# Optimization experiments

Hardware: AMD Instinct MI355X
Metric: run time of the kernel (lower is better)

The kernel has to match this reference:

```python
import jax, jax.numpy as jnp
import numpy as np

DIM = 256; HEADS = 8; HD = DIM // HEADS; WIN = 3; LOCAL = WIN * WIN
SR = 8; SHARED = 4; ROUTED = 2
B = 4; RES = 64; TBL = 4096
EPS = 1.1920929e-07  # torch.finfo(float32).eps


def _l2(x):
    return x / jnp.clip(jnp.linalg.norm(x, axis=-1, keepdims=True), EPS)


def _forward(x, relative_coords_table, q_w, q_b, kv_w, kv_b, temperature,
             query_embedding, rpb_local, learnable_tokens, learnable_bias,
             cpb1_w, cpb1_b, cpb2_w, cpb2_b, sr_w, sr_b, norm_g, norm_b,
             wg_w, wg0_w, wg1_w, proj_w, proj_b, relative_pos_index, H, W):
    B_, N, C = x.shape
    pH, pW = H // SR, W // SR
    PL = pH * pW
    _x = x.reshape(B_ * N, C)

    # ---- MoE head routing: top-k gating over routed heads ----
    gates = jax.nn.softmax(_x @ wg_w.T, axis=1)                 # (BN, n_routed)
    _, idx = jax.lax.top_k(gates, ROUTED)
    mask = jax.nn.one_hot(idx, gates.shape[1], dtype=gates.dtype).sum(axis=1)
    rg = gates * mask
    rg = rg / jnp.clip(jnp.sum(rg, axis=1, keepdims=True), EPS)
    routed_gates = rg.reshape(B_, N, -1) * ROUTED

    # ---- seq-length-scale buffer: log(local valid-window count + pool_len) ----
    r = WIN // 2
    ch = np.minimum(np.arange(H) + r, H - 1) - np.maximum(np.arange(H) - r, 0) + 1
    cw = np.minimum(np.arange(W) + r, W - 1) - np.maximum(np.arange(W) - r, 0) + 1
    sls = jnp.asarray(np.log(np.outer(ch, cw).reshape(-1, 1).astype(np.float32) + PL))

    # ---- queries ----
    q = (x @ q_w.T + q_b).reshape(B_, N, HEADS, HD).transpose(0, 2, 1, 3)
    q_norm = _l2(q)                                             # (B,h,N,d)
    q_scaled = (q_norm + query_embedding) * jax.nn.softplus(temperature) * sls

    # ---- local branch: unfold normalized k and v over 3x3 windows (zero pad) ----
    kv = x @ kv_w.T + kv_b                                      # (B,N,2C)
    k_loc = _l2(kv[..., :C].reshape(B_, N, HEADS, HD)).reshape(B_, N, C)
    kvl = jnp.concatenate([k_loc, kv[..., C:]], -1).transpose(0, 2, 1).reshape(B_, 2 * C, H, W)
    kvp = jnp.pad(kvl, ((0, 0), (0, 0), (r, r), (r, r)))
    patches = jnp.stack([kvp[:, :, i:i + H, j:j + W] for i in range(WIN) for j in range(WIN)], axis=2)
    patches = patches.reshape(B_, 2 * HEADS, HD, LOCAL, N).transpose(0, 1, 4, 2, 3)  # (B,2h,N,d,L)
    k_local, v_local = patches[:, :HEADS], patches[:, HEADS:]

    attn_local = jnp.einsum('bhnd,bhndl->bhnl', q_scaled, k_local) + rpb_local[:, None, :]

    # ---- pooled global branch ----
    x_ = x.transpose(0, 2, 1).reshape(B_, C, H, W)
    x_ = jnp.einsum('oc,bchw->bohw', sr_w, x_) + sr_b[None, :, None, None]  # 1x1 conv
    x_ = jax.nn.gelu(x_, approximate=False)
    x_ = x_.reshape(B_, C, pH, SR, pW, SR).mean((3, 5)).reshape(B_, C, PL).transpose(0, 2, 1)
    mu = x_.mean(-1, keepdims=True)
    var = ((x_ - mu) ** 2).mean(-1, keepdims=True)
    x_ = (x_ - mu) / jnp.sqrt(var + 1e-5) * norm_g + norm_b
    kvp2 = (x_ @ kv_w.T + kv_b).reshape(B_, PL, 2 * HEADS, HD).transpose(0, 2, 1, 3)
    k_pool, v_pool = kvp2[:, :HEADS], kvp2[:, HEADS:]

    cpb = jax.nn.relu(relative_coords_table @ cpb1_w.T + cpb1_b) @ cpb2_w.T + cpb2_b  # (T,h)
    pool_bias = cpb.T[:, relative_pos_index.reshape(-1)].reshape(HEADS, N, PL)
    attn_pool = jnp.einsum('bhnd,bhpd->bhnp', q_scaled, _l2(k_pool)) + pool_bias

    # ---- joint softmax over local + pooled keys ----
    attn = jax.nn.softmax(jnp.concatenate([attn_local, attn_pool], axis=-1), axis=-1)
    a_loc, a_pool = attn[..., :LOCAL], attn[..., LOCAL:]
    a_loc = jnp.einsum('bhnd,hdl->bhnl', q_norm, learnable_tokens) + learnable_bias + a_loc
    x_local = jnp.einsum('bhnl,bhndl->bhnd', a_loc, v_local)
    x_pool = jnp.einsum('bhnp,bhpd->bhnd', a_pool, v_pool)
    out = (x_local + x_pool).transpose(0, 2, 1, 3)              # (B,N,h,d)

    # ---- combine shared + routed head gates ----
    shared_gates = jax.nn.softmax(_x @ wg1_w.T, axis=1).reshape(B_, N, SHARED) * SHARED
    w0 = jax.nn.softmax(_x @ wg0_w.T, axis=1).reshape(B_, N, 2) * 2
    masked = jnp.concatenate([w0[..., 0:1] * shared_gates, w0[..., 1:2] * routed_gates], axis=-1)
    out = (masked[..., None] * out).reshape(B_, N, C)
    return out @ proj_w.T + proj_b


def setup_inputs() -> dict:
    key = jax.random.key(0)
    ks = jax.random.split(key, 20)
    H = W = RES
    N = H * W
    C = DIM
    PL = (H // SR) * (W // SR)

    def nrm(i, shape, s=0.02):
        return jax.random.normal(ks[i], shape, dtype=jnp.float32) * s

    return {
        'x': jax.random.normal(ks[0], (B, N, C), dtype=jnp.float32),
        'relative_coords_table': jax.random.normal(ks[1], (TBL, 2), dtype=jnp.float32),
        'q_w': nrm(3, (C, C)), 'q_b': jnp.zeros((C,), jnp.float32),
        'kv_w': nrm(4, (2 * C, C)), 'kv_b': jnp.zeros((2 * C,), jnp.float32),
        'temperature': jnp.full((HEADS, 1, 1), float(np.log(np.exp(1 / 0.24) - 1)), jnp.float32),
        'query_embedding': nrm(5, (HEADS, 1, HD)),
        'rpb_local': nrm(6, (HEADS, LOCAL), 0.0004),
        'learnable_tokens': nrm(7, (HEADS, HD, LOCAL)),
        'learnable_bias': jnp.zeros((HEADS, 1, LOCAL), jnp.float32),
        'cpb1_w': nrm(8, (512, 2)), 'cpb1_b': jnp.zeros((512,), jnp.float32),
        'cpb2_w': nrm(9, (HEADS, 512)), 'cpb2_b': jnp.zeros((HEADS,), jnp.float32),
        'sr_w': nrm(10, (C, C)), 'sr_b': jnp.zeros((C,), jnp.float32),
        'norm_g': jnp.ones((C,), jnp.float32), 'norm_b': jnp.zeros((C,), jnp.float32),
        'wg_w': nrm(11, (HEADS - SHARED, C)),
        'wg0_w': nrm(12, (2, C)),
        'wg1_w': nrm(13, (SHARED, C)),
        'proj_w': nrm(14, (C, C)), 'proj_b': jnp.zeros((C,), jnp.float32),
        'relative_pos_index': jax.random.randint(ks[2], (N, PL), 0, TBL, dtype=jnp.int32),
        'H': H, 'W': W,
    }


def reference(x, relative_coords_table, q_w, q_b, kv_w, kv_b, temperature,
              query_embedding, rpb_local, learnable_tokens, learnable_bias,
              cpb1_w, cpb1_b, cpb2_w, cpb2_b, sr_w, sr_b, norm_g, norm_b,
              wg_w, wg0_w, wg1_w, proj_w, proj_b, relative_pos_index, H, W):
    return _forward(x, relative_coords_table, q_w, q_b, kv_w, kv_b, temperature,
                    query_embedding, rpb_local, learnable_tokens, learnable_bias,
                    cpb1_w, cpb1_b, cpb2_w, cpb2_b, sr_w, sr_b, norm_g, norm_b,
                    wg_w, wg0_w, wg1_w, proj_w, proj_b, relative_pos_index, H, W)
```

## Files before the change

### kernel.cpp

```cpp
#include <hip/hip_runtime.h>
#include <math.h>

#define EPSF 1.1920929e-07f

typedef __attribute__((ext_vector_type(8))) short short8;
typedef __attribute__((ext_vector_type(4))) float f32x4;

static __device__ __forceinline__ unsigned short f2bf(float f) {
    unsigned int u = __float_as_uint(f);
    return (unsigned short)((u + 0x7FFFu + ((u >> 16) & 1u)) >> 16);
}
static __device__ __forceinline__ float bf2f(unsigned short u) {
    return __uint_as_float((unsigned int)u << 16);
}

__global__ __launch_bounds__(256) void prep_kernel(
    const float* __restrict__ x,
    const float* __restrict__ wg,  const float* __restrict__ wg0,
    const float* __restrict__ wg1,
    const float* __restrict__ q_w, const float* __restrict__ kv_w,
    const float* __restrict__ sr_w, const float* __restrict__ pw,
    const float* __restrict__ tbl,
    const float* __restrict__ c1w, const float* __restrict__ c1b,
    const float* __restrict__ c2w, const float* __restrict__ c2b,
    unsigned short* __restrict__ xbf, float* __restrict__ gate,
    unsigned short* __restrict__ wcat, unsigned short* __restrict__ pwbf,
    float* __restrict__ cpb)
{
    __shared__ float shpad[512];
    const int blk = blockIdx.x;
    const int t   = threadIdx.x;
    if (blk < 4096) {
        const int j = t & 63;
        const int row = (blk << 2) + (t >> 6);
        float4 v = *(const float4*)(x + (size_t)row*256 + j*4);
        ushort4 o;
        o.x = f2bf(v.x); o.y = f2bf(v.y); o.z = f2bf(v.z); o.w = f2bf(v.w);
        *(ushort4*)(xbf + (size_t)row*256 + j*4) = o;
        float d[10];
#pragma unroll
        for (int f = 0; f < 10; ++f) {
            const float* wf = (f < 4) ? (wg + f*256) : (f < 6) ? (wg0 + (f-4)*256)
                                                               : (wg1 + (f-6)*256);
            float4 wv = *(const float4*)(wf + j*4);
            float s = v.x*wv.x + v.y*wv.y + v.z*wv.z + v.w*wv.w;
            s += __shfl_xor(s, 32); s += __shfl_xor(s, 16); s += __shfl_xor(s, 8);
            s += __shfl_xor(s, 4);  s += __shfl_xor(s, 2);  s += __shfl_xor(s, 1);
            d[f] = s;
        }
        if (j == 0) {
            float e[4];
            float m = fmaxf(fmaxf(d[0],d[1]), fmaxf(d[2],d[3]));
            float ssum = 0.f;
            for (int i = 0; i < 4; ++i) { e[i] = expf(d[i]-m); ssum += e[i]; }
            for (int i = 0; i < 4; ++i) e[i] /= ssum;
            int i1 = 0;
            for (int i = 1; i < 4; ++i) if (e[i] > e[i1]) i1 = i;
            int i2 = -1;
            for (int i = 0; i < 4; ++i) if (i != i1 && (i2 < 0 || e[i] > e[i2])) i2 = i;
            float rs = fmaxf(e[i1] + e[i2], EPSF);
            float rg[4] = {0.f,0.f,0.f,0.f};
            rg[i1] = e[i1] / rs * 2.f;
            rg[i2] = e[i2] / rs * 2.f;
            float sh[4];
            float m1 = fmaxf(fmaxf(d[6],d[7]), fmaxf(d[8],d[9]));
            float s1 = 0.f;
            for (int i = 0; i < 4; ++i) { sh[i] = expf(d[6+i]-m1); s1 += sh[i]; }
            float mm = fmaxf(d[4], d[5]);
            float e0 = expf(d[4]-mm), e1 = expf(d[5]-mm);
            float w00 = e0/(e0+e1)*2.f, w01 = e1/(e0+e1)*2.f;
            float* gr = gate + ((size_t)row << 3);
            for (int i = 0; i < 4; ++i) gr[i]   = w00 * (sh[i]/s1*4.f);
            for (int i = 0; i < 4; ++i) gr[4+i] = w01 * rg[i];
        }
    } else if (blk < 4416) {
        const int e = ((blk - 4096)*256 + t)*4;
        if (e < 262144) {
            int n = e >> 8, k = e & 255;
            const float* src = (n < 256) ? (q_w + n*256) :
                               (n < 768) ? (kv_w + (n-256)*256) : (sr_w + (n-768)*256);
            float4 v = *(const float4*)(src + k);
            ushort4 o;
            o.x = f2bf(v.x); o.y = f2bf(v.y); o.z = f2bf(v.z); o.w = f2bf(v.w);
            *(ushort4*)(wcat + e) = o;
        } else {
            int e2 = e - 262144;
            float4 v = *(const float4*)(pw + e2);
            ushort4 o;
            o.x = f2bf(v.x); o.y = f2bf(v.y); o.z = f2bf(v.z); o.w = f2bf(v.w);
            *(ushort4*)(pwbf + e2) = o;
        }
    } else {
        const int r = blk - 4416;
        const float c0 = tbl[(size_t)r*2], c1 = tbl[(size_t)r*2+1];
        for (int i = t; i < 512; i += 256)
            shpad[i] = fmaxf(c0*c1w[i*2] + c1*c1w[i*2+1] + c1b[i], 0.f);
        __syncthreads();
        const int hh = t >> 5, dd = t & 31;
        float s = 0.f;
        for (int i = dd; i < 512; i += 32) s += shpad[i] * c2w[hh*512+i];
        for (int off = 16; off; off >>= 1) s += __shfl_xor(s, off, 32);
        if (dd == 0) cpb[((size_t)r << 3) + hh] = s + c2b[hh];
    }
}

__global__ __launch_bounds__(256) void gemm_mfma(
    const unsigned short* __restrict__ A,
    const unsigned short* __restrict__ W,
    const float* __restrict__ B0, const float* __restrict__ B1,
    const float* __restrict__ B2,
    int r1, int r2, int mode,
    float* __restrict__ C, int ldc,
    unsigned short* __restrict__ qkv,
    const float* __restrict__ temp, const float* __restrict__ qe)
{
    __shared__ __attribute__((aligned(16))) unsigned short At[64*264];
    __shared__ __attribute__((aligned(16))) unsigned short Bt[64*264];
    const int m0 = blockIdx.y << 6;
    const int n0 = blockIdx.x << 6;
    const int t  = threadIdx.x;
    const int w  = t >> 6;
    const int col16 = t & 15;
    const int quad  = (t & 63) >> 4;

    const float* Bp; int noff;
    if (n0 < r1)      { Bp = B0; noff = 0;  }
    else if (n0 < r2) { Bp = B1; noff = r1; }
    else              { Bp = B2; noff = r2; }

    uint4 av[8], bv[8];
#pragma unroll
    for (int j = 0; j < 8; ++j) {
        int ci = j*256 + t;
        int r = ci >> 5, c = ci & 31;
        av[j] = *(const uint4*)(A + (size_t)(m0 + r)*256 + c*8);
        bv[j] = *(const uint4*)(W + (size_t)(n0 + r)*256 + c*8);
    }
#pragma unroll
    for (int j = 0; j < 8; ++j) {
        int ci = j*256 + t;
        int r = ci >> 5, c = ci & 31;
        *(uint4*)(At + r*264 + c*8) = av[j];
        *(uint4*)(Bt + r*264 + c*8) = bv[j];
    }
    __syncthreads();

    f32x4 acc[4];
#pragma unroll
    for (int ct = 0; ct < 4; ++ct) acc[ct] = (f32x4){0.f, 0.f, 0.f, 0.f};
#pragma unroll
    for (int kk = 0; kk < 8; ++kk) {
        short8 af = *(const short8*)(At + (w*16 + col16)*264 + kk*32 + quad*8);
#pragma unroll
        for (int ct = 0; ct < 4; ++ct) {
            short8 bf = *(const short8*)(Bt + (ct*16 + col16)*264 + kk*32 + quad*8);
            acc[ct] = __builtin_amdgcn_mfma_f32_16x16x32_bf16(af, bf, acc[ct], 0, 0, 0);
        }
    }

    float bias_c[4];
#pragma unroll
    for (int ct = 0; ct < 4; ++ct)
        bias_c[ct] = Bp[n0 + ct*16 + col16 - noff];

    if (mode == 0) {
        const int region = n0 >> 8;
        float qe_c[4], spt_c[4];
        if (region == 0) {
#pragma unroll
            for (int c = 0; c < 4; ++c) {
                int col = n0 + c*16 + col16;
                spt_c[c] = log1pf(expf(temp[(col >> 5) & 7]));
                qe_c[c]  = qe[col];
            }
        }
#pragma unroll
        for (int reg = 0; reg < 4; ++reg) {
            const int row = m0 + w*16 + quad*4 + reg;
            float v[4];
#pragma unroll
            for (int c = 0; c < 4; ++c) v[c] = acc[c][reg] + bias_c[c];
            if (region <= 1) {
#pragma unroll
                for (int hp = 0; hp < 2; ++hp) {
                    float s = v[2*hp]*v[2*hp] + v[2*hp+1]*v[2*hp+1];
                    s += __shfl_xor(s, 1); s += __shfl_xor(s, 2);
                    s += __shfl_xor(s, 4); s += __shfl_xor(s, 8);
                    float inv = 1.0f / fmaxf(sqrtf(s), EPSF);
                    v[2*hp]   *= inv;
                    v[2*hp+1] *= inv;
                }
            }
            if (region == 0) {
                int n = row & 4095;
                int y = n >> 6, x = n & 63;
                int cy = (y == 0 || y == 63) ? 2 : 3;
                int cx = (x == 0 || x == 63) ? 2 : 3;
                float sls = logf((float)(cy*cx) + 64.0f);
#pragma unroll
                for (int c = 0; c < 4; ++c)
                    v[c] = (v[c] + qe_c[c]) * (spt_c[c] * sls);
            }
            if (region == 3) {
#pragma unroll
                for (int c = 0; c < 4; ++c) {
                    float g = 0.5f * v[c] * (1.0f + erff(v[c] * 0.70710678118654752f));
                    C[(size_t)row * ldc + n0 + c*16 + col16] = g;
                }
            } else {
#pragma unroll
                for (int c = 0; c < 4; ++c)
                    qkv[(size_t)row * 2048 + n0 + c*16 + col16] = f2bf(v[c]);
            }
        }
    } else {
#pragma unroll
        for (int reg = 0; reg < 4; ++reg) {
            const int row = m0 + w*16 + quad*4 + reg;
#pragma unroll
            for (int c = 0; c < 4; ++c)
                C[(size_t)row * ldc + n0 + c*16 + col16] = acc[c][reg] + bias_c[c];
        }
    }
}

__global__ __launch_bounds__(256) void poolkv_kernel(
    const float* __restrict__ buf,
    const float* __restrict__ g, const float* __restrict__ bb,
    const float* __restrict__ kv_w, const float* __restrict__ kv_b,
    unsigned short* __restrict__ kpb, unsigned short* __restrict__ vpb)
{
    __shared__ float r1[256], r2[256];
    __shared__ float xs[256];
    __shared__ float rowv[512];
    __shared__ float inv[8];
    const int blk = blockIdx.x;
    const int b = blk >> 6, p = blk & 63;
    const int py = p >> 3, px = p & 7;
    const int t = threadIdx.x;
    float acc = 0.f;
    for (int dy = 0; dy < 8; ++dy)
#pragma unroll
        for (int dx = 0; dx < 8; ++dx) {
            int s = ((py*8+dy) << 6) + px*8 + dx;
            acc += buf[(((size_t)(b*4096+s)) << 10) + 768 + t];
        }
    acc *= (1.0f/64.0f);
    r1[t] = acc; r2[t] = acc*acc;
    __syncthreads();
    for (int off = 128; off; off >>= 1) {
        if (t < off) { r1[t] += r1[t+off]; r2[t] += r2[t+off]; }
        __syncthreads();
    }
    float mu  = r1[0] * (1.0f/256.0f);
    float var = r2[0] * (1.0f/256.0f) - mu*mu;
    float rstd = rsqrtf(var + 1e-5f);
    xs[t] = (acc - mu) * rstd * g[t] + bb[t];
    __syncthreads();
    for (int o = t; o < 512; o += 256) {
        const float* wr = kv_w + ((size_t)o << 8);
        float s = kv_b[o];
        for (int k = 0; k < 256; ++k) s += xs[k]*wr[k];
        rowv[o] = s;
    }
    __syncthreads();
    if (t < 8) {
        float s = 0.f;
        for (int dd = 0; dd < 32; ++dd) { float v = rowv[t*32+dd]; s += v*v; }
        inv[t] = 1.0f / fmaxf(sqrtf(s), EPSF);
    }
    __syncthreads();
    const int h = t >> 5;
    size_t o = ((((size_t)(b*8+h))*64 + p) << 5) + (t & 31);
    kpb[o] = f2bf(rowv[t] * inv[h]);
    vpb[o] = f2bf(rowv[256 + t]);
}

__global__ __launch_bounds__(256, 4) void attn_mfma(
    const unsigned short* __restrict__ qkv,
    unsigned short* __restrict__ ao,
    const unsigned short* __restrict__ kpb,
    const unsigned short* __restrict__ vpb,
    const float* __restrict__ cpb,
    const int*   __restrict__ rpi,
    const float* __restrict__ temp,
    const float* __restrict__ qe,
    const float* __restrict__ rpb,
    const float* __restrict__ lt,
    const float* __restrict__ lb,
    const float* __restrict__ gate)
{
    __shared__ __attribute__((aligned(16))) unsigned short U0[112*40];
    __shared__ __attribute__((aligned(16))) unsigned short U1[64*40];
    __shared__ __attribute__((aligned(16))) unsigned short QS[64*40];
    __shared__ __attribute__((aligned(16))) unsigned short P[64*136];
    __shared__ __attribute__((aligned(16))) unsigned short LTT[16*40];
    __shared__ float invscL[64], gateL[64], rpbL[9], dqvL[16];
    __shared__ int hofs[112];

    const int tile = blockIdx.x;
    const int h    = blockIdx.y;
    const int b    = blockIdx.z;
    const int ty0  = (tile >> 3) << 3;
    const int tx0  = (tile & 7) << 3;
    const int t    = threadIdx.x;

    const float spt = log1pf(expf(temp[h]));
    if (t < 64) {
        int y = ty0 + (t >> 3), x = tx0 + (t & 7);
        int cy = (y == 0 || y == 63) ? 2 : 3;
        int cx = (x == 0 || x == 63) ? 2 : 3;
        invscL[t] = 1.0f / (spt * logf((float)(cy*cx) + 64.0f));
        gateL[t] = gate[(((size_t)(b*4096 + ((y<<6)|x))) << 3) + h];
    } else if (t < 80) {
        int j = t - 64;
        float s = 0.f;
        if (j < 9) {
            s = lb[h*9 + j];
            for (int dd = 0; dd < 32; ++dd)
                s -= qe[h*32+dd] * lt[(h*32+dd)*9 + j];
        }
        dqvL[j] = s;
    } else if (t < 89) {
        rpbL[t-80] = rpb[h*9 + (t-80)];
    } else if (t >= 128 && t < 240) {
        int r = t - 128;
        int off = -1;
        if (r < 100) {
            int y = ty0 + r/10 - 1, x = tx0 + r%10 - 1;
            if (y >= 0 && y < 64 && x >= 0 && x < 64)
                off = (b*4096 + ((y<<6)|x))*2048 + h*32;
        }
        hofs[r] = off;
        if (r >= 100) hofs[r] = -1;
    }
    for (int i = t; i < 16*32; i += 256) {
        int j = i >> 5, dd = i & 31;
        LTT[j*40 + dd] = (j < 9) ? f2bf(lt[(h*32+dd)*9 + j]) : (unsigned short)0;
    }
    __syncthreads();

    unsigned short* KH = U0;
    unsigned short* KP = U1;
    for (int i = t; i < 112*8; i += 256) {
        int r = i >> 3, sg = i & 7;
        int off = hofs[r];
        uint2 val = {0u, 0u};
        if (off >= 0)
            val = *(const uint2*)(qkv + (size_t)off + 256 + sg*4);
        *(uint2*)(KH + r*40 + sg*4) = val;
    }
    {
        const unsigned short* src = kpb + (size_t)(b*8+h)*2048;
        for (int i = t; i < 512; i += 256)
            *(uint2*)(KP + (i >> 3)*40 + (i & 7)*4) = *(const uint2*)(src + i*4);
    }
    for (int i = t; i < 512; i += 256) {
        int n = i >> 3, sg = i & 7;
        int off = hofs[(n >> 3)*10 + (n & 7) + 11];
        *(uint2*)(QS + n*40 + sg*4) = *(const uint2*)(qkv + (size_t)off + sg*4);
    }
    __syncthreads();

    const int lane  = t & 63;
    const int w     = t >> 6;
    const int col16 = lane & 15;
    const int quad  = lane >> 4;
    const int s_w   = (20*w) & ~15;

    float pbias[4][4];
#pragma unroll
    for (int ct = 0; ct < 4; ++ct) {
        int p = ct*16 + col16;
#pragma unroll
        for (int reg = 0; reg < 4; ++reg) {
            int n = w*16 + quad*4 + reg;
            int y = ty0 + (n >> 3), x = tx0 + (n & 7);
            int ngl = (y << 6) | x;
            pbias[ct][reg] = cpb[((size_t)rpi[(size_t)ngl*64 + p] << 3) + h];
        }
    }

    short8 aq = *(const short8*)(QS + (w*16 + col16)*40 + quad*8);
    f32x4 cl[4], cp[4];
    {
        const f32x4 z = {0.f, 0.f, 0.f, 0.f};
#pragma unroll
        for (int ct = 0; ct < 4; ++ct) {
            short8 bk = *(const short8*)(KH + (s_w + ct*16 + col16)*40 + quad*8);
            cl[ct] = __builtin_amdgcn_mfma_f32_16x16x32_bf16(aq, bk, z, 0, 0, 0);
        }
#pragma unroll
        for (int ct = 0; ct < 4; ++ct) {
            short8 bp = *(const short8*)(KP + (ct*16 + col16)*40 + quad*8);
            cp[ct] = __builtin_amdgcn_mfma_f32_16x16x32_bf16(aq, bp, z, 0, 0, 0);
        }
    }
#pragma unroll
    for (int ct = 0; ct < 4; ++ct) {
        int hk = s_w + ct*16 + col16;
        int ky = hk / 10, kx = hk - ky*10;
#pragma unroll
        for (int reg = 0; reg < 4; ++reg) {
            int n = w*16 + quad*4 + reg;
            int dy = ky - (n >> 3), dx = kx - (n & 7);
            bool valid = (dy >= 0 && dy <= 2 && dx >= 0 && dx <= 2);
            cl[ct][reg] = valid ? (cl[ct][reg] + rpbL[dy*3 + dx]) : -1e30f;
        }
    }
#pragma unroll
    for (int ct = 0; ct < 4; ++ct)
#pragma unroll
        for (int reg = 0; reg < 4; ++reg)
            cp[ct][reg] += pbias[ct][reg];
    float inv[4];
#pragma unroll
    for (int reg = 0; reg < 4; ++reg) {
        float m = -1e30f;
#pragma unroll
        for (int ct = 0; ct < 4; ++ct) m = fmaxf(m, cl[ct][reg]);
#pragma unroll
        for (int ct = 0; ct < 4; ++ct) m = fmaxf(m, cp[ct][reg]);
        m = fmaxf(m, __shfl_xor(m, 1)); m = fmaxf(m, __shfl_xor(m, 2));
        m = fmaxf(m, __shfl_xor(m, 4)); m = fmaxf(m, __shfl_xor(m, 8));
        float s = 0.f;
#pragma unroll
        for (int ct = 0; ct < 4; ++ct) {
            float e = __builtin_expf(cl[ct][reg] - m); cl[ct][reg] = e; s += e;
        }
#pragma unroll
        for (int ct = 0; ct < 4; ++ct) {
            float e = __builtin_expf(cp[ct][reg] - m); cp[ct][reg] = e; s += e;
        }
        s += __shfl_xor(s, 1); s += __shfl_xor(s, 2);
        s += __shfl_xor(s, 4); s += __shfl_xor(s, 8);
        inv[reg] = 1.0f / s;
    }
#pragma unroll
    for (int ct = 0; ct < 4; ++ct)
#pragma unroll
        for (int reg = 0; reg < 4; ++reg) {
            int n = w*16 + quad*4 + reg;
            P[n*136 + ct*16 + col16] = f2bf(cl[ct][reg] * inv[reg]);
        }
#pragma unroll
    for (int ct = 0; ct < 4; ++ct)
#pragma unroll
        for (int reg = 0; reg < 4; ++reg) {
            int n = w*16 + quad*4 + reg;
            P[n*136 + 64 + ct*16 + col16] = f2bf(cp[ct][reg] * inv[reg]);
        }
    {
        const f32x4 z = {0.f, 0.f, 0.f, 0.f};
        short8 blt = *(const short8*)(LTT + col16*40 + quad*8);
        f32x4 cd = __builtin_amdgcn_mfma_f32_16x16x32_bf16(aq, blt, z, 0, 0, 0);
        if (col16 < 9) {
            int dy = col16 / 3, dx = col16 - dy*3;
#pragma unroll
            for (int reg = 0; reg < 4; ++reg) {
                int n = w*16 + quad*4 + reg;
                float ltv = cd[reg] * invscL[n] + dqvL[col16];
                int hk = ((n >> 3) + dy)*10 + (n & 7) + dx;
                int pc = hk - s_w;
                P[n*136 + pc] = f2bf(bf2f(P[n*136 + pc]) + ltv);
            }
        }
    }
    __syncthreads();

    unsigned short* VT  = U0;
    unsigned short* VPT = U1;
    for (int i = t; i < 1792; i += 256) {
        int rlo = i & 15, rest = i >> 4;
        int dp = rest & 15, r = (rest >> 4)*16 + rlo;
        int off = hofs[r];
        unsigned val = 0;
        if (off >= 0)
            val = *(const unsigned*)(qkv + (size_t)off + 512 + dp*2);
        VT[(2*dp)*136 + r]   = (unsigned short)(val & 0xffffu);
        VT[(2*dp+1)*136 + r] = (unsigned short)(val >> 16);
    }
    for (int i = t; i < 1024; i += 256) {
        int plo = i & 15, rest = i >> 4;
        int dp = rest & 15, p = (rest >> 4)*16 + plo;
        unsigned val = *(const unsigned*)(vpb + (size_t)(b*8+h)*2048 + p*32 + dp*2);
        VPT[(2*dp)*72 + p]   = (unsigned short)(val & 0xffffu);
        VPT[(2*dp+1)*72 + p] = (unsigned short)(val >> 16);
    }
    __syncthreads();

    f32x4 o0 = {0.f,0.f,0.f,0.f}, o1 = {0.f,0.f,0.f,0.f};
#pragma unroll
    for (int ks = 0; ks < 4; ++ks) {
        short8 a = *(const short8*)(P + (w*16 + col16)*136 + ks*32 + quad*8);
        short8 b0, b1;
        if (ks < 2) {
            b0 = *(const short8*)(VT + col16*136      + s_w + ks*32 + quad*8);
            b1 = *(const short8*)(VT + (16+col16)*136 + s_w + ks*32 + quad*8);
        } else {
            b0 = *(const short8*)(VPT + col16*72      + (ks-2)*32 + quad*8);
            b1 = *(const short8*)(VPT + (16+col16)*72 + (ks-2)*32 + quad*8);
        }
        o0 = __builtin_amdgcn_mfma_f32_16x16x32_bf16(a, b0, o0, 0, 0, 0);
        o1 = __builtin_amdgcn_mfma_f32_16x16x32_bf16(a, b1, o1, 0, 0, 0);
    }
#pragma unroll
    for (int reg = 0; reg < 4; ++reg) {
        int n = w*16 + quad*4 + reg;
        int y = ty0 + (n >> 3), x = tx0 + (n & 7);
        size_t rowo = (size_t)(b*4096 + ((y<<6)|x))*256 + h*32;
        float g = gateL[n];
        ao[rowo + col16]      = f2bf(o0[reg] * g);
        ao[rowo + 16 + col16] = f2bf(o1[reg] * g);
    }
}

extern "C" void kernel_launch(void* const* d_in, const int* in_sizes, int n_in,
                              void* d_out, int out_size, void* d_ws, size_t ws_size,
                              hipStream_t stream)
{
    const float* x    = (const float*)d_in[0];
    const float* tbl  = (const float*)d_in[1];
    const float* q_w  = (const float*)d_in[2];
    const float* q_b  = (const float*)d_in[3];
    const float* kv_w = (const float*)d_in[4];
    const float* kv_b = (const float*)d_in[5];
    const float* temp = (const float*)d_in[6];
    const float* qe   = (const float*)d_in[7];
    const float* rpb  = (const float*)d_in[8];
    const float* lt   = (const float*)d_in[9];
    const float* lb   = (const float*)d_in[10];
    const float* c1w  = (const float*)d_in[11];
    const float* c1b  = (const float*)d_in[12];
    const float* c2w  = (const float*)d_in[13];
    const float* c2b  = (const float*)d_in[14];
    const float* sr_w = (const float*)d_in[15];
    const float* sr_b = (const float*)d_in[16];
    const float* ng   = (const float*)d_in[17];
    const float* nbias= (const float*)d_in[18];
    const float* wg   = (const float*)d_in[19];
    const float* wg0  = (const float*)d_in[20];
    const float* wg1  = (const float*)d_in[21];
    const float* pw   = (const float*)d_in[22];
    const float* pb   = (const float*)d_in[23];
    const int*   rpi  = (const int*)d_in[24];
    (void)in_sizes; (void)n_in; (void)out_size; (void)ws_size;

    float* buf   = (float*)d_ws;
    unsigned short* qkvb = (unsigned short*)d_ws;
    float* xp    = buf + (size_t)16384*1024;
    float* kpoolf= xp + 65536;
    unsigned short* kpb = (unsigned short*)kpoolf;
    unsigned short* vpb = kpb + 131072;
    float* cpbb  = kpoolf + 131072;
    float* gateb = cpbb + 32768;
    unsigned short* xbf  = (unsigned short*)(gateb + 131072);
    unsigned short* ao   = xbf;
    unsigned short* wcat = xbf + (size_t)16384*256;
    unsigned short* pwbf = wcat + 262144;
    float* out   = (float*)d_out;

    prep_kernel<<<8512,256,0,stream>>>(x, wg, wg0, wg1, q_w, kv_w, sr_w, pw,
                                       tbl, c1w, c1b, c2w, c2b,
                                       xbf, gateb, wcat, pwbf, cpbb);
    gemm_mfma<<<dim3(16,256),256,0,stream>>>(xbf, wcat, q_b, kv_b, sr_b,
                                             256, 768, 0, buf, 1024,
                                             qkvb, temp, qe);
    poolkv_kernel<<<256,256,0,stream>>>(buf, ng, nbias, kv_w, kv_b, kpb, vpb);
    attn_mfma<<<dim3(64,8,4),256,0,stream>>>(qkvb, ao, kpb, vpb, cpbb, rpi,
                                             temp, qe, rpb, lt, lb, gateb);
    gemm_mfma<<<dim3(4,256),256,0,stream>>>(ao, pwbf, pb, pb, pb,
                                            1<<30, 1<<30, 1, out, 256,
                                            (unsigned short*)nullptr, nullptr, nullptr);
}
```

Measured before the change: 260.3 us.

## Keep A tile in registers and loop over N with double-buffered weight tiles

The GEMM kernel now gives each block a 64-row slab of A, held in registers, and loops over all N column tiles. Weight tiles are double-buffered in shared memory, with the next tile prefetched during the MFMA work. This removes repeated A loads across column blocks, but cuts the grid to 256 blocks, which may leave CUs underused. Separately, kv_w is transposed in the prep kernel so the pooled-KV projection reads coalesced weights instead of strided per-thread rows.

```diff
diff --git a/kernel.cpp b/kernel.cpp
--- a/kernel.cpp
+++ b/kernel.cpp
@@ -25,7 +25,7 @@
     const float* __restrict__ c2w, const float* __restrict__ c2b,
     unsigned short* __restrict__ xbf, float* __restrict__ gate,
     unsigned short* __restrict__ wcat, unsigned short* __restrict__ pwbf,
-    float* __restrict__ cpb)
+    float* __restrict__ kv_wT, float* __restrict__ cpb)
 {
     __shared__ float shpad[512];
     const int blk = blockIdx.x;
@@ -90,8 +90,16 @@
             o.x = f2bf(v.x); o.y = f2bf(v.y); o.z = f2bf(v.z); o.w = f2bf(v.w);
             *(ushort4*)(pwbf + e2) = o;
         }
+    } else if (blk < 4544) {
+        const int e = ((blk - 4416)*256 + t)*4;
+        int o = e >> 8, k = e & 255;
+        float4 v = *(const float4*)(kv_w + e);
+        kv_wT[(k+0)*512 + o] = v.x;
+        kv_wT[(k+1)*512 + o] = v.y;
+        kv_wT[(k+2)*512 + o] = v.z;
+        kv_wT[(k+3)*512 + o] = v.w;
     } else {
-        const int r = blk - 4416;
+        const int r = blk - 4544;
         const float c0 = tbl[(size_t)r*2], c1 = tbl[(size_t)r*2+1];
         for (int i = t; i < 512; i += 256)
             shpad[i] = fmaxf(c0*c1w[i*2] + c1*c1w[i*2+1] + c1b[i], 0.f);
@@ -104,122 +112,148 @@
     }
 }
 
-__global__ __launch_bounds__(256) void gemm_mfma(
+__global__ __launch_bounds__(256) void gemm_nloop(
     const unsigned short* __restrict__ A,
     const unsigned short* __restrict__ W,
     const float* __restrict__ B0, const float* __restrict__ B1,
     const float* __restrict__ B2,
-    int r1, int r2, int mode,
+    int r1, int r2, int nTotal, int mode,
     float* __restrict__ C, int ldc,
     unsigned short* __restrict__ qkv,
     const float* __restrict__ temp, const float* __restrict__ qe)
 {
-    __shared__ __attribute__((aligned(16))) unsigned short At[64*264];
-    __shared__ __attribute__((aligned(16))) unsigned short Bt[64*264];
-    const int m0 = blockIdx.y << 6;
-    const int n0 = blockIdx.x << 6;
+    __shared__ __attribute__((aligned(16))) unsigned short Bt[2][64*264];
+    const int m0 = blockIdx.x << 6;
     const int t  = threadIdx.x;
     const int w  = t >> 6;
     const int col16 = t & 15;
     const int quad  = (t & 63) >> 4;
 
-    const float* Bp; int noff;
-    if (n0 < r1)      { Bp = B0; noff = 0;  }
-    else if (n0 < r2) { Bp = B1; noff = r1; }
-    else              { Bp = B2; noff = r2; }
-
-    uint4 av[8], bv[8];
+    short8 afr[8];
+    {
+        const unsigned short* ap = A + (size_t)(m0 + w*16 + col16)*256 + quad*8;
+#pragma unroll
+        for (int kk = 0; kk < 8; ++kk)
+            afr[kk] = *(const short8*)(ap + kk*32);
+    }
+    float sls_r[4];
+    if (mode == 0) {
+#pragma unroll
+        for (int reg = 0; reg < 4; ++reg) {
+            int row = (m0 + w*16 + quad*4 + reg) & 4095;
+            int y = row >> 6, x = row & 63;
+            int cy = (y == 0 || y == 63) ? 2 : 3;
+            int cx = (x == 0 || x == 63) ? 2 : 3;
+            sls_r[reg] = logf((float)(cy*cx) + 64.0f);
+        }
+    }
+
+    const int NC = nTotal >> 6;
+    uint4 stg[8];
 #pragma unroll
     for (int j = 0; j < 8; ++j) {
         int ci = j*256 + t;
-        int r = ci >> 5, c = ci & 31;
-        av[j] = *(const uint4*)(A + (size_t)(m0 + r)*256 + c*8);
-        bv[j] = *(const uint4*)(W + (size_t)(n0 + r)*256 + c*8);
+        stg[j] = *(const uint4*)(W + (size_t)(ci >> 5)*256 + (ci & 31)*8);
     }
 #pragma unroll
     for (int j = 0; j < 8; ++j) {
         int ci = j*256 + t;
-        int r = ci >> 5, c = ci & 31;
-        *(uint4*)(At + r*264 + c*8) = av[j];
-        *(uint4*)(Bt + r*264 + c*8) = bv[j];
-    }
-    __syncthreads();
-
-    f32x4 acc[4];
-#pragma unroll
-    for (int ct = 0; ct < 4; ++ct) acc[ct] = (f32x4){0.f, 0.f, 0.f, 0.f};
-#pragma unroll
-    for (int kk = 0; kk < 8; ++kk) {
-        short8 af = *(const short8*)(At + (w*16 + col16)*264 + kk*32 + quad*8);
-#pragma unroll
-        for (int ct = 0; ct < 4; ++ct) {
-            short8 bf = *(const short8*)(Bt + (ct*16 + col16)*264 + kk*32 + quad*8);
-            acc[ct] = __builtin_amdgcn_mfma_f32_16x16x32_bf16(af, bf, acc[ct], 0, 0, 0);
-        }
-    }
-
-    float bias_c[4];
-#pragma unroll
-    for (int ct = 0; ct < 4; ++ct)
-        bias_c[ct] = Bp[n0 + ct*16 + col16 - noff];
-
-    if (mode == 0) {
-        const int region = n0 >> 8;
-        float qe_c[4], spt_c[4];
-        if (region == 0) {
-#pragma unroll
-            for (int c = 0; c < 4; ++c) {
-                int col = n0 + c*16 + col16;
-                spt_c[c] = log1pf(expf(temp[(col >> 5) & 7]));
-                qe_c[c]  = qe[col];
+        *(uint4*)(&Bt[0][(ci >> 5)*264 + (ci & 31)*8]) = stg[j];
+    }
+
+    for (int nc = 0; nc < NC; ++nc) {
+        const int cur = nc & 1;
+        __syncthreads();
+        if (nc + 1 < NC) {
+            const unsigned short* wp = W + (size_t)(nc + 1)*64*256;
+#pragma unroll
+            for (int j = 0; j < 8; ++j) {
+                int ci = j*256 + t;
+                stg[j] = *(const uint4*)(wp + (size_t)(ci >> 5)*256 + (ci & 31)*8);
             }
         }
-#pragma unroll
-        for (int reg = 0; reg < 4; ++reg) {
-            const int row = m0 + w*16 + quad*4 + reg;
-            float v[4];
-#pragma unroll
-            for (int c = 0; c < 4; ++c) v[c] = acc[c][reg] + bias_c[c];
-            if (region <= 1) {
-#pragma unroll
-                for (int hp = 0; hp < 2; ++hp) {
-                    float s = v[2*hp]*v[2*hp] + v[2*hp+1]*v[2*hp+1];
-                    s += __shfl_xor(s, 1); s += __shfl_xor(s, 2);
-                    s += __shfl_xor(s, 4); s += __shfl_xor(s, 8);
-                    float inv = 1.0f / fmaxf(sqrtf(s), EPSF);
-                    v[2*hp]   *= inv;
-                    v[2*hp+1] *= inv;
+        f32x4 acc[4];
+#pragma unroll
+        for (int ct = 0; ct < 4; ++ct) acc[ct] = (f32x4){0.f, 0.f, 0.f, 0.f};
+#pragma unroll
+        for (int kk = 0; kk < 8; ++kk) {
+#pragma unroll
+            for (int ct = 0; ct < 4; ++ct) {
+                short8 bf = *(const short8*)(&Bt[cur][(ct*16 + col16)*264 + kk*32 + quad*8]);
+                acc[ct] = __builtin_amdgcn_mfma_f32_16x16x32_bf16(afr[kk], bf, acc[ct], 0, 0, 0);
+            }
+        }
+        if (nc + 1 < NC) {
+#pragma unroll
+            for (int j = 0; j < 8; ++j) {
+                int ci = j*256 + t;
+                *(uint4*)(&Bt[cur ^ 1][(ci >> 5)*264 + (ci & 31)*8]) = stg[j];
+            }
+        }
+
+        const int n0 = nc << 6;
+        const float* Bp; int noff;
+        if (n0 < r1)      { Bp = B0; noff = 0;  }
+        else if (n0 < r2) { Bp = B1; noff = r1; }
+        else              { Bp = B2; noff = r2; }
+        float bias_c[4];
+#pragma unroll
+        for (int c = 0; c < 4; ++c)
+            bias_c[c] = Bp[n0 + c*16 + col16 - noff];
+
+        if (mode == 0) {
+            const int region = n0 >> 8;
+            float qe_c[4], spt_c[4];
+            if (region == 0) {
+#pragma unroll
+                for (int c = 0; c < 4; ++c) {
+                    int col = n0 + c*16 + col16;
+                    spt_c[c] = log1pf(expf(temp[(col >> 5) & 7]));
+                    qe_c[c]  = qe[col];
                 }
             }
-            if (region == 0) {
-                int n = row & 4095;
-                int y = n >> 6, x = n & 63;
-                int cy = (y == 0 || y == 63) ? 2 : 3;
-                int cx = (x == 0 || x == 63) ? 2 : 3;
-                float sls = logf((float)(cy*cx) + 64.0f);
+#pragma unroll
+            for (int reg = 0; reg < 4; ++reg) {
+                const int row = m0 + w*16 + quad*4 + reg;
+                float v[4];
+#pragma unroll
+                for (int c = 0; c < 4; ++c) v[c] = acc[c][reg] + bias_c[c];
+                if (region <= 1) {
+#pragma unroll
+                    for (int hp = 0; hp < 2; ++hp) {
+                        float s = v[2*hp]*v[2*hp] + v[2*hp+1]*v[2*hp+1];
+                        s += __shfl_xor(s, 1); s += __shfl_xor(s, 2);
+                        s += __shfl_xor(s, 4); s += __shfl_xor(s, 8);
+                        float inv = 1.0f / fmaxf(sqrtf(s), EPSF);
+                        v[2*hp]   *= inv;
+                        v[2*hp+1] *= inv;
+                    }
+                }
+                if (region == 0) {
+#pragma unroll
+                    for (int c = 0; c < 4; ++c)
+                        v[c] = (v[c] + qe_c[c]) * (spt_c[c] * sls_r[reg]);
+                }
+                if (region == 3) {
+#pragma unroll
+                    for (int c = 0; c < 4; ++c) {
+                        float g = 0.5f * v[c] * (1.0f + erff(v[c] * 0.70710678118654752f));
+                        C[(size_t)row * ldc + n0 + c*16 + col16] = g;
+                    }
+                } else {
+#pragma unroll
+                    for (int c = 0; c < 4; ++c)
+                        qkv[(size_t)row * 2048 + n0 + c*16 + col16] = f2bf(v[c]);
+                }
+            }
+        } else {
+#pragma unroll
+            for (int reg = 0; reg < 4; ++reg) {
+                const int row = m0 + w*16 + quad*4 + reg;
 #pragma unroll
                 for (int c = 0; c < 4; ++c)
-                    v[c] = (v[c] + qe_c[c]) * (spt_c[c] * sls);
+                    C[(size_t)row * ldc + n0 + c*16 + col16] = acc[c][reg] + bias_c[c];
             }
-            if (region == 3) {
-#pragma unroll
-                for (int c = 0; c < 4; ++c) {
-                    float g = 0.5f * v[c] * (1.0f + erff(v[c] * 0.70710678118654752f));
-                    C[(size_t)row * ldc + n0 + c*16 + col16] = g;
-                }
-            } else {
-#pragma unroll
-                for (int c = 0; c < 4; ++c)
-                    qkv[(size_t)row * 2048 + n0 + c*16 + col16] = f2bf(v[c]);
-            }
-        }
-    } else {
-#pragma unroll
-        for (int reg = 0; reg < 4; ++reg) {
-            const int row = m0 + w*16 + quad*4 + reg;
-#pragma unroll
-            for (int c = 0; c < 4; ++c)
-                C[(size_t)row * ldc + n0 + c*16 + col16] = acc[c][reg] + bias_c[c];
         }
     }
 }
@@ -227,7 +261,7 @@
 __global__ __launch_bounds__(256) void poolkv_kernel(
     const float* __restrict__ buf,
     const float* __restrict__ g, const float* __restrict__ bb,
-    const float* __restrict__ kv_w, const float* __restrict__ kv_b,
+    const float* __restrict__ kv_wT, const float* __restrict__ kv_b,
     unsigned short* __restrict__ kpb, unsigned short* __restrict__ vpb)
 {
     __shared__ float r1[256], r2[256];
@@ -257,11 +291,16 @@
     float rstd = rsqrtf(var + 1e-5f);
     xs[t] = (acc - mu) * rstd * g[t] + bb[t];
     __syncthreads();
-    for (int o = t; o < 512; o += 256) {
-        const float* wr = kv_w + ((size_t)o << 8);
-        float s = kv_b[o];
-        for (int k = 0; k < 256; ++k) s += xs[k]*wr[k];
-        rowv[o] = s;
+    {
+        float s0 = kv_b[t], s1 = kv_b[256 + t];
+#pragma unroll 4
+        for (int k = 0; k < 256; ++k) {
+            float xv = xs[k];
+            const float* wr = kv_wT + (size_t)k*512;
+            s0 += xv * wr[t];
+            s1 += xv * wr[256 + t];
+        }
+        rowv[t] = s0; rowv[256 + t] = s1;
     }
     __syncthreads();
     if (t < 8) {
@@ -332,7 +371,6 @@
                 off = (b*4096 + ((y<<6)|x))*2048 + h*32;
         }
         hofs[r] = off;
-        if (r >= 100) hofs[r] = -1;
     }
     for (int i = t; i < 16*32; i += 256) {
         int j = i >> 5, dd = i & 31;
@@ -554,22 +592,23 @@
     unsigned short* vpb = kpb + 131072;
     float* cpbb  = kpoolf + 131072;
     float* gateb = cpbb + 32768;
-    unsigned short* xbf  = (unsigned short*)(gateb + 131072);
+    float* kvwT  = gateb + 131072;
+    unsigned short* xbf  = (unsigned short*)(kvwT + 131072);
     unsigned short* ao   = xbf;
     unsigned short* wcat = xbf + (size_t)16384*256;
     unsigned short* pwbf = wcat + 262144;
     float* out   = (float*)d_out;
 
-    prep_kernel<<<8512,256,0,stream>>>(x, wg, wg0, wg1, q_w, kv_w, sr_w, pw,
+    prep_kernel<<<8640,256,0,stream>>>(x, wg, wg0, wg1, q_w, kv_w, sr_w, pw,
                                        tbl, c1w, c1b, c2w, c2b,
-                                       xbf, gateb, wcat, pwbf, cpbb);
-    gemm_mfma<<<dim3(16,256),256,0,stream>>>(xbf, wcat, q_b, kv_b, sr_b,
-                                             256, 768, 0, buf, 1024,
-                                             qkvb, temp, qe);
-    poolkv_kernel<<<256,256,0,stream>>>(buf, ng, nbias, kv_w, kv_b, kpb, vpb);
+                                       xbf, gateb, wcat, pwbf, kvwT, cpbb);
+    gemm_nloop<<<256,256,0,stream>>>(xbf, wcat, q_b, kv_b, sr_b,
+                                     256, 768, 1024, 0, buf, 1024,
+                                     qkvb, temp, qe);
+    poolkv_kernel<<<256,256,0,stream>>>(buf, ng, nbias, kvwT, kv_b, kpb, vpb);
     attn_mfma<<<dim3(64,8,4),256,0,stream>>>(qkvb, ao, kpb, vpb, cpbb, rpi,
                                              temp, qe, rpb, lt, lb, gateb);
-    gemm_mfma<<<dim3(4,256),256,0,stream>>>(ao, pwbf, pb, pb, pb,
-                                            1<<30, 1<<30, 1, out, 256,
-                                            (unsigned short*)nullptr, nullptr, nullptr);
+    gemm_nloop<<<256,256,0,stream>>>(ao, pwbf, pb, pb, pb,
+                                     1<<30, 1<<30, 256, 1, out, 256,
+                                     (unsigned short*)nullptr, nullptr, nullptr);
 }
```

Measured after the change: 295.0 us. 1.13x slower.
